# Kernel optimization log

Hardware: AMD Instinct MI355X
Metric: run time of the kernel (lower is better)

The kernel has to match this reference:

```python
import jax, jax.numpy as jnp
import numpy as np

N = 3600      # nodes (pinned by h0/c0 shape in the torch module)
H = 512       # lstm_hidden
PES = 588     # pes feature width (LSTM input size)
PROT = 384    # protein feature width
OC = 256      # out_channels
E = 230400    # edges (avg degree 64)


def _lstm_cell(x, h, c, wih, whh, bih, bhh):
    # single-timestep PyTorch LSTM cell; gate order i, f, g, o
    g = x @ wih.T + h @ whh.T + bih + bhh
    i, f, gg, o = jnp.split(g, 4, axis=-1)
    c2 = jax.nn.sigmoid(f) * c + jax.nn.sigmoid(i) * jnp.tanh(gg)
    return jax.nn.sigmoid(o) * jnp.tanh(c2)


def _gcn(x, rows, cols, norm, W, b):
    # PyG GCNConv: X' = D^{-1/2}(A+I)D^{-1/2} X W + b
    xw = x @ W
    return jax.ops.segment_sum(xw[rows] * norm[:, None], cols, num_segments=N) + b


def setup_inputs() -> dict:
    key = jax.random.key(0)
    ks = jax.random.split(key, 24)
    s = 0.05
    d = {
        "x": jax.random.normal(ks[0], (N, PES + PROT), jnp.float32),
        "edge_index": jax.random.randint(ks[1], (2, E), 0, N),
        "h0": jax.random.normal(ks[2], (4, N, H), jnp.float32),
        "c0": jax.random.normal(ks[3], (4, N, H), jnp.float32),
    }
    ins = [PES, PES, 2 * H, 2 * H]
    names = ["l0f", "l0b", "l1f", "l1b"]
    for i, (nm, di) in enumerate(zip(names, ins)):
        d["wih" + nm] = jax.random.normal(ks[4 + 4 * i], (4 * H, di), jnp.float32) * s
        d["whh" + nm] = jax.random.normal(ks[5 + 4 * i], (4 * H, H), jnp.float32) * s
        d["bih" + nm] = jnp.zeros((4 * H,), jnp.float32)
        d["bhh" + nm] = jnp.zeros((4 * H,), jnp.float32)
    d["W1"] = jax.random.normal(ks[20], (PROT + 2 * H, 2 * OC), jnp.float32) * s
    d["b1"] = jnp.zeros((2 * OC,), jnp.float32)
    d["W2"] = jax.random.normal(ks[21], (2 * OC, OC), jnp.float32) * s
    d["b2"] = jnp.zeros((OC,), jnp.float32)
    return d


def reference(x, edge_index, h0, c0,
              wihl0f, whhl0f, bihl0f, bhhl0f,
              wihl0b, whhl0b, bihl0b, bhhl0b,
              wihl1f, whhl1f, bihl1f, bhhl1f,
              wihl1b, whhl1b, bihl1b, bhhl1b,
              W1, b1, W2, b2):
    pes = x[:, :PES]
    prot = x[:, PES:]
    # BiLSTM over seq_len=1: one cell step per direction per layer
    hf = _lstm_cell(pes, h0[0], c0[0], wihl0f, whhl0f, bihl0f, bhhl0f)
    hb = _lstm_cell(pes, h0[1], c0[1], wihl0b, whhl0b, bihl0b, bhhl0b)
    x1 = jnp.concatenate([hf, hb], axis=1)
    hf2 = _lstm_cell(x1, h0[2], c0[2], wihl1f, whhl1f, bihl1f, bhhl1f)
    hb2 = _lstm_cell(x1, h0[3], c0[3], wihl1b, whhl1b, bihl1b, bhhl1b)
    x_p = jnp.concatenate([hf2, hb2], axis=1) / 100.0
    feat = jnp.concatenate([prot, x_p], axis=1)  # dropout is identity in eval
    # add self-loops, symmetric normalization
    loop = jnp.arange(N)
    rows = jnp.concatenate([edge_index[0], loop])
    cols = jnp.concatenate([edge_index[1], loop])
    deg = jax.ops.segment_sum(jnp.ones_like(rows, jnp.float32), cols, num_segments=N)
    dinv = jax.lax.rsqrt(deg)  # deg >= 1 because of self-loops
    norm = dinv[rows] * dinv[cols]
    h1 = jax.nn.relu(_gcn(feat, rows, cols, norm, W1, b1))
    return _gcn(h1, rows, cols, norm, W2, b2)
```

## Files before the change

kernel.cpp:

```cpp
#include <hip/hip_runtime.h>
#include <hip/hip_bf16.h>

#define NN 3600
#define MP 3712
#define KADJ 3616
#define NH (3600*512)
#define EE 230400
#define NKT0 9
#define NKT1 12

typedef __hip_bfloat16 bf16;
typedef __bf16 bf16x8 __attribute__((ext_vector_type(8)));
typedef float f32x4 __attribute__((ext_vector_type(4)));
typedef int i32x8 __attribute__((ext_vector_type(8)));
typedef unsigned char u8x16 __attribute__((ext_vector_type(16)));

typedef __attribute__((address_space(1))) void as1v;
typedef __attribute__((address_space(3))) void as3v;

__device__ __forceinline__ void glds16(void* lds, const void* g) {
  __builtin_amdgcn_global_load_lds((as1v*)(void*)g, (as3v*)lds, 16, 0, 0);
}

__device__ __forceinline__ float sigm(float v) { return 1.0f / (1.0f + expf(-v)); }

__device__ __forceinline__ unsigned char f2fp8(float f) {
  return (unsigned char)(__builtin_amdgcn_cvt_pk_fp8_f32(f, 0.f, 0, false) & 0xff);
}

template<int MODE>
__global__ __launch_bounds__(256) void gemm_lstm8(
    const unsigned char* __restrict__ Af, const unsigned char* __restrict__ Bf,
    const float* __restrict__ c0f, const float* __restrict__ bihf,
    const float* __restrict__ bhhf,
    const unsigned char* __restrict__ Ab, const unsigned char* __restrict__ Bb,
    const float* __restrict__ c0b, const float* __restrict__ bihb,
    const float* __restrict__ bhhb,
    void* __restrict__ dst1, void* __restrict__ dst2,
    int nkt, int hx)
{
  __shared__ alignas(16) unsigned char smem[65536];
  const bool back = (int)blockIdx.x >= hx;
  const unsigned char* A = back ? Ab : Af;
  const unsigned char* B = back ? Bb : Bf;
  const float* c0  = back ? c0b : c0f;
  const float* bih = back ? bihb : bihf;
  const float* bhh = back ? bhhb : bhhf;
  const int t = threadIdx.x, w = t >> 6, l = t & 63;
  const int nblk = back ? (int)blockIdx.x - hx : (int)blockIdx.x;
  const unsigned char* gA = A + (((size_t)blockIdx.y * nkt) << 14) + t*16;
  const unsigned char* gB = B + (((size_t)nblk * nkt) << 14) + t*16;
  const int wm = (w>>1)*64, wn = (w&1)*64;
  const int kb = l >> 4;
  const int aoff = kb*4096 + (wm + (l&15))*32;
  const int boff = 16384 + kb*4096 + (wn + (l&15))*32;
  f32x4 acc[4][4] = {};

  auto STAGE = [&](int buf, int kt) {
    unsigned char* lA = smem + buf*32768 + w*1024;
    unsigned char* lB = smem + buf*32768 + 16384 + w*1024;
    const size_t ko = (size_t)kt << 14;
    glds16(lA,          gA + ko);
    glds16(lA + 4096,   gA + ko + 4096);
    glds16(lA + 8192,   gA + ko + 8192);
    glds16(lA + 12288,  gA + ko + 12288);
    glds16(lB,          gB + ko);
    glds16(lB + 4096,   gB + ko + 4096);
    glds16(lB + 8192,   gB + ko + 8192);
    glds16(lB + 12288,  gB + ko + 12288);
  };

  STAGE(0, 0);
  __syncthreads();
  int cur = 0;
  for (int kt = 0; kt < nkt; ++kt) {
    if (kt + 1 < nkt) STAGE(cur ^ 1, kt + 1);
    const unsigned char* base = smem + cur*32768;
    i32x8 av[4], bv[4];
#pragma unroll
    for (int mi = 0; mi < 4; ++mi) av[mi] = *(const i32x8*)(base + aoff + mi*512);
#pragma unroll
    for (int ni = 0; ni < 4; ++ni) bv[ni] = *(const i32x8*)(base + boff + ni*512);
#pragma unroll
    for (int mi = 0; mi < 4; ++mi)
#pragma unroll
      for (int ni = 0; ni < 4; ++ni)
        acc[mi][ni] = __builtin_amdgcn_mfma_scale_f32_16x16x128_f8f6f4(
            av[mi], bv[ni], acc[mi][ni], 0, 0, 0, 127, 0, 127);
    __syncthreads();
    cur ^= 1;
  }
  const int jh = (((nblk << 7) + wn) >> 2) + (l & 15);
  const float bI = bih[jh]        + bhh[jh];
  const float bF = bih[512 + jh]  + bhh[512 + jh];
  const float bG = bih[1024 + jh] + bhh[1024 + jh];
  const float bO = bih[1536 + jh] + bhh[1536 + jh];
  const int crow = ((int)blockIdx.y << 7) + wm + ((l>>4)<<2);
  const int kk = (back ? 512 : 0) + jh;
  const size_t kpart = ((size_t)(kk >> 7) << 14) + ((size_t)((kk >> 5) & 3) << 12) + (kk & 31);
  const int colOff = back ? 896 : 384;
#pragma unroll
  for (int mi = 0; mi < 4; ++mi)
#pragma unroll
    for (int jr = 0; jr < 4; ++jr) {
      const int n = crow + mi*16 + jr;
      if (n < NN) {
        const float gi = acc[mi][0][jr] + bI;
        const float gf = acc[mi][1][jr] + bF;
        const float gg = acc[mi][2][jr] + bG;
        const float go = acc[mi][3][jr] + bO;
        const float c2 = sigm(gf) * c0[(size_t)n*512 + jh] + sigm(gi) * tanhf(gg);
        const float h  = sigm(go) * tanhf(c2);
        if (MODE == 0) {
          const unsigned char h8 = f2fp8(h);
          const size_t off = (((size_t)(n >> 7) * NKT1) << 14) + kpart + ((size_t)(n & 127) << 5);
          ((unsigned char*)dst1)[off] = h8;
          ((unsigned char*)dst2)[off] = h8;
        } else {
          ((bf16*)dst1)[(size_t)n*1408 + colOff + jh] = __float2bfloat16(h * 0.01f);
        }
      }
    }
}

__global__ __launch_bounds__(256) void gemm_bt_sk(const bf16* __restrict__ A,
                                                  const bf16* __restrict__ B,
                                                  float* __restrict__ Cp,
                                                  int Kp, int ldc, int ksteps)
{
  __shared__ alignas(16) char smem[32768];
  const int t = threadIdx.x, w = t >> 6, l = t & 63;
  const int mbase = blockIdx.y << 7, nbase = blockIdx.x << 7;
  const int total = Kp >> 5;
  const int kstart = blockIdx.z * ksteps;
  int steps = total - kstart; if (steps > ksteps) steps = ksteps;
  const size_t ldb = (size_t)Kp * 2;
  const char* gA = (const char*)A + (size_t)(mbase + w*16 + (l>>2)) * ldb
                   + (size_t)((l&3)*16) + (size_t)kstart*64;
  const char* gB = (const char*)B + (size_t)(nbase + w*16 + (l>>2)) * ldb
                   + (size_t)((l&3)*16) + (size_t)kstart*64;
  const int wm = (w>>1)*64, wn = (w&1)*64;
  const int aoff = (wm + (l&15))*64 + (l>>4)*16;
  const int boff = 8192 + (wn + (l&15))*64 + (l>>4)*16;
  f32x4 acc[4][4] = {};
  const size_t chunk = ldb * 64;

  auto STAGE = [&](int buf, int kt) {
    char* lA = smem + buf*16384 + w*1024;
    char* lB = smem + buf*16384 + 8192 + w*1024;
    const size_t ko = (size_t)kt * 64;
    glds16(lA,        gA + ko);
    glds16(lA + 4096, gA + ko + chunk);
    glds16(lB,        gB + ko);
    glds16(lB + 4096, gB + ko + chunk);
  };

  STAGE(0, 0);
  __syncthreads();
  int cur = 0;
  for (int kt = 0; kt < steps; ++kt) {
    if (kt + 1 < steps) STAGE(cur ^ 1, kt + 1);
    const char* base = smem + cur*16384;
    bf16x8 av[4], bv[4];
#pragma unroll
    for (int mi = 0; mi < 4; ++mi) av[mi] = *(const bf16x8*)(base + aoff + mi*1024);
#pragma unroll
    for (int ni = 0; ni < 4; ++ni) bv[ni] = *(const bf16x8*)(base + boff + ni*1024);
#pragma unroll
    for (int mi = 0; mi < 4; ++mi)
#pragma unroll
      for (int ni = 0; ni < 4; ++ni)
        acc[mi][ni] = __builtin_amdgcn_mfma_f32_16x16x32_bf16(av[mi], bv[ni], acc[mi][ni], 0, 0, 0);
    __syncthreads();
    cur ^= 1;
  }
  float* Cz = Cp + (size_t)blockIdx.z * ((size_t)(gridDim.y << 7) * ldc);
  const int crow = mbase + wm + ((l>>4)<<2);
  const int ccol = nbase + wn + (l&15);
#pragma unroll
  for (int mi = 0; mi < 4; ++mi)
#pragma unroll
    for (int ni = 0; ni < 4; ++ni) {
      float* cp = Cz + (size_t)(crow + mi*16)*ldc + (ccol + ni*16);
#pragma unroll
      for (int j = 0; j < 4; ++j) cp[(size_t)j*ldc] = acc[mi][ni][j];
    }
}

__global__ void reduce_bf_pad(const float* __restrict__ p, bf16* __restrict__ dst, int Z)
{
  int k = blockIdx.x*256 + threadIdx.x;
  int r = blockIdx.y;
  if (k >= KADJ) return;
  const size_t psz = (size_t)gridDim.y * MP;
  float s = 0.f;
  if (k < NN)
    for (int z = 0; z < Z; ++z) s += p[(size_t)z*psz + (size_t)r*MP + k];
  dst[(size_t)r*KADJ + k] = __float2bfloat16(s);
}

__global__ void reduce_relu_bf(const float* __restrict__ p, const float* __restrict__ b,
                               bf16* __restrict__ dst)
{
  int idx = blockIdx.x*256 + threadIdx.x;
  int f = idx & 511;
  float s = b[f];
#pragma unroll
  for (int z = 0; z < 4; ++z) s += p[(size_t)z*MP*512 + idx];
  dst[idx] = __float2bfloat16(fmaxf(s, 0.f));
}

__global__ void reduce_bias_out(const float* __restrict__ p, const float* __restrict__ b,
                                float* __restrict__ out)
{
  int idx = blockIdx.x*256 + threadIdx.x;
  if (idx >= NN*256) return;
  int f = idx & 255;
  float s = b[f];
#pragma unroll
  for (int z = 0; z < 8; ++z) s += p[(size_t)z*MP*256 + idx];
  out[idx] = s;
}

__global__ void pack_B_8(const float* __restrict__ wih, const float* __restrict__ whh,
                         unsigned char* __restrict__ dst, int kx, int nkt)
{
  const int kt = blockIdx.x >> 2, kbId = blockIdx.x & 3;
  const int t = threadIdx.x;
  const int r = t >> 1, kio = (t & 1) << 4;
  const int R = ((int)blockIdx.y << 7) + r;
  const int src = (((R >> 4) & 3) << 9) + ((R >> 6) << 4) + (R & 15);
  const int kbase = kt*128 + kbId*32 + kio;
  u8x16 v;
#pragma unroll
  for (int i = 0; i < 16; ++i) {
    const int k = kbase + i;
    float f = 0.f;
    if (k < kx) f = wih[(size_t)src*kx + k];
    else if (k < kx + 512) f = whh[(size_t)src*512 + (k - kx)];
    v[i] = f2fp8(f);
  }
  *(u8x16*)(dst + (((size_t)blockIdx.y*nkt + kt) << 14) + (kbId << 12) + (r << 5) + kio) = v;
}

__global__ void pack_A0_8(const float* __restrict__ x, const float* __restrict__ h0,
                          unsigned char* __restrict__ a0f, unsigned char* __restrict__ a0b)
{
  const int kt = blockIdx.x >> 2, kbId = blockIdx.x & 3;
  const int t = threadIdx.x;
  const int r = t >> 1, kio = (t & 1) << 4;
  const int n = ((int)blockIdx.y << 7) + r;
  const int kbase = kt*128 + kbId*32 + kio;
  const float* hsrc = h0 + (size_t)blockIdx.z * NH;
  u8x16 v;
#pragma unroll
  for (int i = 0; i < 16; ++i) {
    const int k = kbase + i;
    float f = 0.f;
    if (n < NN) {
      if (k < 588) f = x[(size_t)n*972 + k];
      else if (k < 1100) f = hsrc[(size_t)n*512 + (k - 588)];
    }
    v[i] = f2fp8(f);
  }
  unsigned char* dst = blockIdx.z ? a0b : a0f;
  *(u8x16*)(dst + (((size_t)blockIdx.y*NKT0 + kt) << 14) + (kbId << 12) + (r << 5) + kio) = v;
}

__global__ void pack_A1h_8(const float* __restrict__ h0,
                           unsigned char* __restrict__ a1f, unsigned char* __restrict__ a1b)
{
  const int kt = 8 + (blockIdx.x >> 2), kbId = blockIdx.x & 3;
  const int t = threadIdx.x;
  const int r = t >> 1, kio = (t & 1) << 4;
  const int n = ((int)blockIdx.y << 7) + r;
  const int kbase = kt*128 + kbId*32 + kio;
  const float* hsrc = h0 + (size_t)(2 + blockIdx.z) * NH;
  u8x16 v;
#pragma unroll
  for (int i = 0; i < 16; ++i) {
    const int k = kbase + i;
    float f = (n < NN) ? hsrc[(size_t)n*512 + (k - 1024)] : 0.f;
    v[i] = f2fp8(f);
  }
  unsigned char* dst = blockIdx.z ? a1b : a1f;
  *(u8x16*)(dst + (((size_t)blockIdx.y*NKT1 + kt) << 14) + (kbId << 12) + (r << 5) + kio) = v;
}

__global__ void pack_BT(const float* __restrict__ W, bf16* __restrict__ dst, int Nc, int K)
{
  int k = blockIdx.x*256 + threadIdx.x;
  int n = blockIdx.y;
  if (k >= K) return;
  dst[(size_t)n*K + k] = __float2bfloat16(W[(size_t)k*Nc + n]);
}

__global__ void pack_prot(const float* __restrict__ x, bf16* __restrict__ afeat)
{
  int k = blockIdx.x*256 + threadIdx.x;
  int n = blockIdx.y;
  if (k >= 384) return;
  float v = (n < NN) ? x[(size_t)n*972 + 588 + k] : 0.f;
  afeat[(size_t)n*1408 + k] = __float2bfloat16(v);
}

__global__ void deg_count(const int* __restrict__ ecols, int* __restrict__ deg)
{
  int e = blockIdx.x*256 + threadIdx.x;
  if (e < EE) atomicAdd(&deg[ecols[e]], 1);
}

__global__ void calc_dinv(const int* __restrict__ deg, float* __restrict__ dinv)
{
  int n = blockIdx.x*256 + threadIdx.x;
  if (n < NN) dinv[n] = 1.0f / sqrtf((float)(deg[n] + 1));
}

__global__ void adj_scatter(const int* __restrict__ er, const int* __restrict__ ec,
                            const float* __restrict__ dinv, float* __restrict__ adjf)
{
  int e = blockIdx.x*256 + threadIdx.x;
  if (e < EE) {
    int r = er[e], c = ec[e];
    atomicAdd(&adjf[(size_t)c*KADJ + r], dinv[r]*dinv[c]);
  } else if (e < EE + NN) {
    int n = e - EE;
    float d = dinv[n];
    atomicAdd(&adjf[(size_t)n*KADJ + n], d*d);
  }
}

__global__ void cvt_bf(const float* __restrict__ src, int lds,
                       bf16* __restrict__ dst, int rv, int kv)
{
  int k = blockIdx.x*256 + threadIdx.x;
  int r = blockIdx.y;
  if (k >= KADJ) return;
  float v = (r < rv && k < kv) ? src[(size_t)r*lds + k] : 0.f;
  dst[(size_t)r*KADJ + k] = __float2bfloat16(v);
}

#define OFF_DEG   ((size_t)0)
#define OFF_DINV  ((size_t)16384)
#define OFF_BW2   ((size_t)32768)
#define OFF_B0F   ((size_t)294912)
#define OFF_B0B   ((size_t)4882432)
#define OFF_B1F   ((size_t)9469952)
#define OFF_B1B   ((size_t)15761408)
#define OFF_BW1   ((size_t)22052864)
#define OFF_A0F   ((size_t)23494656)
#define OFF_A0B   ((size_t)31809536)
#define OFF_A1F   ((size_t)40124416)
#define OFF_A1B   ((size_t)51527680)
#define OFF_G     ((size_t)62930944)
#define OFF_AFEAT OFF_A0F
#define OFF_XW1P  OFF_G
#define OFF_XWT1B OFF_B0F
#define OFF_ADJF  ((size_t)40124416)
#define OFF_ADJB  ((size_t)4194304)
#define OFF_H1P   ((size_t)40124416)
#define OFF_H1    ((size_t)70533120)
#define OFF_XW2P  ((size_t)74334208)
#define OFF_XWT2B ((size_t)89538560)
#define OFF_O2P   ((size_t)40124416)

extern "C" void kernel_launch(void* const* d_in, const int* in_sizes, int n_in,
                              void* d_out, int out_size, void* d_ws, size_t ws_size,
                              hipStream_t stream)
{
  const float* x    = (const float*)d_in[0];
  const int*   ei   = (const int*)d_in[1];
  const float* h0   = (const float*)d_in[2];
  const float* c0   = (const float*)d_in[3];
  const float* wih0f = (const float*)d_in[4];
  const float* whh0f = (const float*)d_in[5];
  const float* bih0f = (const float*)d_in[6];
  const float* bhh0f = (const float*)d_in[7];
  const float* wih0b = (const float*)d_in[8];
  const float* whh0b = (const float*)d_in[9];
  const float* bih0b = (const float*)d_in[10];
  const float* bhh0b = (const float*)d_in[11];
  const float* wih1f = (const float*)d_in[12];
  const float* whh1f = (const float*)d_in[13];
  const float* bih1f = (const float*)d_in[14];
  const float* bhh1f = (const float*)d_in[15];
  const float* wih1b = (const float*)d_in[16];
  const float* whh1b = (const float*)d_in[17];
  const float* bih1b = (const float*)d_in[18];
  const float* bhh1b = (const float*)d_in[19];
  const float* W1 = (const float*)d_in[20];
  const float* b1 = (const float*)d_in[21];
  const float* W2 = (const float*)d_in[22];
  const float* b2 = (const float*)d_in[23];

  char* ws = (char*)d_ws;
  int*   deg  = (int*)(ws + OFF_DEG);
  float* dinv = (float*)(ws + OFF_DINV);
  unsigned char* B0f8 = (unsigned char*)(ws + OFF_B0F);
  unsigned char* B0b8 = (unsigned char*)(ws + OFF_B0B);
  unsigned char* B1f8 = (unsigned char*)(ws + OFF_B1F);
  unsigned char* B1b8 = (unsigned char*)(ws + OFF_B1B);
  bf16* BW1 = (bf16*)(ws + OFF_BW1);
  bf16* BW2 = (bf16*)(ws + OFF_BW2);
  unsigned char* A0f8 = (unsigned char*)(ws + OFF_A0F);
  unsigned char* A0b8 = (unsigned char*)(ws + OFF_A0B);
  unsigned char* A1f8 = (unsigned char*)(ws + OFF_A1F);
  unsigned char* A1b8 = (unsigned char*)(ws + OFF_A1B);
  bf16* Afeat = (bf16*)(ws + OFF_AFEAT);
  float* xw1p  = (float*)(ws + OFF_XW1P);
  bf16*  xwt1b = (bf16*)(ws + OFF_XWT1B);
  float* adjf  = (float*)(ws + OFF_ADJF);
  bf16*  adjb  = (bf16*)(ws + OFF_ADJB);
  float* h1p   = (float*)(ws + OFF_H1P);
  bf16*  h1bf  = (bf16*)(ws + OFF_H1);
  float* xw2p  = (float*)(ws + OFF_XW2P);
  bf16*  xwt2b = (bf16*)(ws + OFF_XWT2B);
  float* o2p   = (float*)(ws + OFF_O2P);
  float* outp = (float*)d_out;

  hipMemsetAsync(deg, 0, (size_t)NN*4, stream);
  deg_count<<<dim3((EE+255)/256), 256, 0, stream>>>(ei + EE, deg);
  calc_dinv<<<dim3(15), 256, 0, stream>>>(deg, dinv);

  pack_B_8<<<dim3(NKT0*4, 16), 256, 0, stream>>>(wih0f, whh0f, B0f8, 588, NKT0);
  pack_B_8<<<dim3(NKT0*4, 16), 256, 0, stream>>>(wih0b, whh0b, B0b8, 588, NKT0);
  pack_B_8<<<dim3(NKT1*4, 16), 256, 0, stream>>>(wih1f, whh1f, B1f8, 1024, NKT1);
  pack_B_8<<<dim3(NKT1*4, 16), 256, 0, stream>>>(wih1b, whh1b, B1b8, 1024, NKT1);
  pack_BT<<<dim3(6, 512), 256, 0, stream>>>(W1, BW1, 512, 1408);
  pack_BT<<<dim3(2, 256), 256, 0, stream>>>(W2, BW2, 256, 512);

  pack_A0_8<<<dim3(NKT0*4, 29, 2), 256, 0, stream>>>(x, h0, A0f8, A0b8);
  pack_A1h_8<<<dim3(16, 29, 2), 256, 0, stream>>>(h0, A1f8, A1b8);

  gemm_lstm8<0><<<dim3(32, 29), 256, 0, stream>>>(
      A0f8, B0f8, c0,              bih0f, bhh0f,
      A0b8, B0b8, c0 + (size_t)NH, bih0b, bhh0b,
      A1f8, A1b8, NKT0, 16);

  pack_prot<<<dim3(2, MP), 256, 0, stream>>>(x, Afeat);

  gemm_lstm8<1><<<dim3(32, 29), 256, 0, stream>>>(
      A1f8, B1f8, c0 + (size_t)2*NH, bih1f, bhh1f,
      A1b8, B1b8, c0 + (size_t)3*NH, bih1b, bhh1b,
      Afeat, nullptr, NKT1, 16);

  gemm_bt_sk<<<dim3(29, 4, 4), 256, 0, stream>>>(BW1, Afeat, xw1p, 1408, MP, 11);
  reduce_bf_pad<<<dim3(15, 512), 256, 0, stream>>>(xw1p, xwt1b, 4);

  hipMemsetAsync(adjf, 0, (size_t)NN*KADJ*4, stream);
  adj_scatter<<<dim3((EE+NN+255)/256), 256, 0, stream>>>(ei, ei + EE, dinv, adjf);
  cvt_bf<<<dim3(15, MP), 256, 0, stream>>>(adjf, KADJ, adjb, NN, KADJ);

  gemm_bt_sk<<<dim3(4, 29, 4), 256, 0, stream>>>(adjb, xwt1b, h1p, KADJ, 512, 29);
  reduce_relu_bf<<<dim3(MP*512/256), 256, 0, stream>>>(h1p, b1, h1bf);

  gemm_bt_sk<<<dim3(29, 2, 4), 256, 0, stream>>>(BW2, h1bf, xw2p, 512, MP, 4);
  reduce_bf_pad<<<dim3(15, 256), 256, 0, stream>>>(xw2p, xwt2b, 4);

  gemm_bt_sk<<<dim3(2, 29, 8), 256, 0, stream>>>(adjb, xwt2b, o2p, KADJ, 256, 15);
  reduce_bias_out<<<dim3(3600), 256, 0, stream>>>(o2p, b2, outp);
}
```

Baseline: 341.4 us.

## Deepen GEMM prefetch with partial vmcnt waits and swizzle LSTM block order

Both GEMM main loops now issue loads two k-tiles ahead and wait with s_waitcnt vmcnt(N), so only the older stage must land before each barrier. The aim is to keep global-to-LDS copies in flight while the MFMAs run. The LSTM GEMM also remaps block IDs with a swizzle so that nearby blocks share A/B tiles, which should improve L2 reuse. The risks are that hand-counted vmcnt values depend on exactly how many loads are outstanding, and that the swizzle hardcodes a 32x116 grid.

```diff
diff --git a/kernel.cpp b/kernel.cpp
--- a/kernel.cpp
+++ b/kernel.cpp
@@ -40,15 +40,18 @@
     int nkt, int hx)
 {
   __shared__ alignas(16) unsigned char smem[65536];
-  const bool back = (int)blockIdx.x >= hx;
+  const int id  = (int)blockIdx.y * 32 + (int)blockIdx.x;
+  const int swz = (id & 7) * 116 + (id >> 3);
+  const int bx  = swz & 31, by = swz >> 5;
+  const bool back = bx >= hx;
   const unsigned char* A = back ? Ab : Af;
   const unsigned char* B = back ? Bb : Bf;
   const float* c0  = back ? c0b : c0f;
   const float* bih = back ? bihb : bihf;
   const float* bhh = back ? bhhb : bhhf;
   const int t = threadIdx.x, w = t >> 6, l = t & 63;
-  const int nblk = back ? (int)blockIdx.x - hx : (int)blockIdx.x;
-  const unsigned char* gA = A + (((size_t)blockIdx.y * nkt) << 14) + t*16;
+  const int nblk = back ? bx - hx : bx;
+  const unsigned char* gA = A + (((size_t)by * nkt) << 14) + t*16;
   const unsigned char* gB = B + (((size_t)nblk * nkt) << 14) + t*16;
   const int wm = (w>>1)*64, wn = (w&1)*64;
   const int kb = l >> 4;
@@ -71,10 +74,14 @@
   };
 
   STAGE(0, 0);
-  __syncthreads();
+  STAGE(1, 1);
   int cur = 0;
   for (int kt = 0; kt < nkt; ++kt) {
-    if (kt + 1 < nkt) STAGE(cur ^ 1, kt + 1);
+    if (kt + 1 < nkt) asm volatile("s_waitcnt vmcnt(8)" ::: "memory");
+    else              asm volatile("s_waitcnt vmcnt(0)" ::: "memory");
+    __builtin_amdgcn_sched_barrier(0);
+    __builtin_amdgcn_s_barrier();
+    __builtin_amdgcn_sched_barrier(0);
     const unsigned char* base = smem + cur*32768;
     i32x8 av[4], bv[4];
 #pragma unroll
@@ -87,7 +94,10 @@
       for (int ni = 0; ni < 4; ++ni)
         acc[mi][ni] = __builtin_amdgcn_mfma_scale_f32_16x16x128_f8f6f4(
             av[mi], bv[ni], acc[mi][ni], 0, 0, 0, 127, 0, 127);
-    __syncthreads();
+    __builtin_amdgcn_sched_barrier(0);
+    __builtin_amdgcn_s_barrier();
+    __builtin_amdgcn_sched_barrier(0);
+    if (kt + 2 < nkt) STAGE(cur, kt + 2);
     cur ^= 1;
   }
   const int jh = (((nblk << 7) + wn) >> 2) + (l & 15);
@@ -95,7 +105,7 @@
   const float bF = bih[512 + jh]  + bhh[512 + jh];
   const float bG = bih[1024 + jh] + bhh[1024 + jh];
   const float bO = bih[1536 + jh] + bhh[1536 + jh];
-  const int crow = ((int)blockIdx.y << 7) + wm + ((l>>4)<<2);
+  const int crow = (by << 7) + wm + ((l>>4)<<2);
   const int kk = (back ? 512 : 0) + jh;
   const size_t kpart = ((size_t)(kk >> 7) << 14) + ((size_t)((kk >> 5) & 3) << 12) + (kk & 31);
   const int colOff = back ? 896 : 384;
@@ -156,10 +166,14 @@
   };
 
   STAGE(0, 0);
-  __syncthreads();
+  if (steps > 1) STAGE(1, 1);
   int cur = 0;
   for (int kt = 0; kt < steps; ++kt) {
-    if (kt + 1 < steps) STAGE(cur ^ 1, kt + 1);
+    if (kt + 1 < steps) asm volatile("s_waitcnt vmcnt(4)" ::: "memory");
+    else                asm volatile("s_waitcnt vmcnt(0)" ::: "memory");
+    __builtin_amdgcn_sched_barrier(0);
+    __builtin_amdgcn_s_barrier();
+    __builtin_amdgcn_sched_barrier(0);
     const char* base = smem + cur*16384;
     bf16x8 av[4], bv[4];
 #pragma unroll
@@ -171,7 +185,10 @@
 #pragma unroll
       for (int ni = 0; ni < 4; ++ni)
         acc[mi][ni] = __builtin_amdgcn_mfma_f32_16x16x32_bf16(av[mi], bv[ni], acc[mi][ni], 0, 0, 0);
-    __syncthreads();
+    __builtin_amdgcn_sched_barrier(0);
+    __builtin_amdgcn_s_barrier();
+    __builtin_amdgcn_sched_barrier(0);
+    if (kt + 2 < steps) STAGE(cur, kt + 2);
     cur ^= 1;
   }
   float* Cz = Cp + (size_t)blockIdx.z * ((size_t)(gridDim.y << 7) * ldc);
```

Measured after the change: 332.5 us. 1.03x faster.
